# Kernel optimization log

Measured on AMD Instinct MI355X. Metric: run time of the kernel, lower is better.

## Reference

```python
import jax, jax.numpy as jnp
import numpy as np

SCALES = (1, 3, 7, 15)
EPS_LN = 1e-5

def _layernorm(x, g, b):
    mu = jnp.mean(x, axis=-1, keepdims=True)
    var = jnp.mean(jnp.square(x - mu), axis=-1, keepdims=True)
    return (x - mu) / jnp.sqrt(var + EPS_LN) * g + b

def setup_inputs() -> dict:
    key = jax.random.key(0)
    ks = jax.random.split(key, 6)
    B, L, H, NL = 8, 4096, 1024, 4
    s = 0.02
    return {
        "sequence_features": jax.random.normal(ks[0], (B, L, H), jnp.float32),
        "hierarchy_masks": jax.random.uniform(ks[1], (B, L, NL), jnp.float32),
        "level_embeddings": jax.random.normal(ks[2], (NL, H), jnp.float32) * s,
        "lt_w": jax.random.normal(ks[3], (H, H), jnp.float32) * (1.0 / np.sqrt(H)),
        "lt_b": jnp.zeros((H,), jnp.float32),
        "ln1_g": jnp.ones((H,), jnp.float32),
        "ln1_b": jnp.zeros((H,), jnp.float32),
        "ft_w": jax.random.normal(ks[4], (H, H), jnp.float32) * (1.0 / np.sqrt(H)),
        "ft_b": jnp.zeros((H,), jnp.float32),
        "ln2_g": jnp.ones((H,), jnp.float32),
        "ln2_b": jnp.zeros((H,), jnp.float32),
    }

def _hierarchical_fusion(t, masks, level_emb, temperature=1.0):
    # t: [B,L,H], masks: [B,L,NL], level_emb: [NL,H]
    H = t.shape[-1]
    scores = jnp.einsum('blh,nh->bln', t, level_emb) / temperature      # [B,L,NL]
    keep = masks > 0.5
    w = jnp.where(keep, jnp.exp(scores), 0.0)                            # masked exp weights
    tot = jnp.sum(w, axis=-1, keepdims=True)                             # [B,L,1]
    fused = jnp.einsum('bln,nh->blh', w, level_emb)
    fused = jnp.where(tot > 1e-8, fused / jnp.where(tot > 1e-8, tot, 1.0), fused)
    gate = jax.nn.sigmoid(jnp.sum(fused * t, axis=-1, keepdims=True) / H)
    return gate * fused + (1.0 - gate) * t

def _multi_scale(x):
    # x: [B,L,H]; variable-window mean per scale via prefix sums
    B, L, H = x.shape
    csum = jnp.concatenate([jnp.zeros((B, 1, H), x.dtype), jnp.cumsum(x, axis=1)], axis=1)  # [B,L+1,H]
    pos = jnp.arange(L)
    agg = jnp.zeros_like(x)
    for scale in SCALES:
        start = jnp.clip(pos - scale // 2, 0, L)
        end = jnp.clip(pos + scale // 2 + 1, 0, L)
        wsum = jnp.take(csum, end, axis=1) - jnp.take(csum, start, axis=1)  # [B,L,H]
        cnt = (end - start).astype(x.dtype)[None, :, None]
        sw = 1.0 / (1.0 + np.log(float(scale)))
        agg = agg + sw * (wsum / cnt)
    return agg

def reference(sequence_features, hierarchy_masks, level_embeddings, lt_w, lt_b,
              ln1_g, ln1_b, ft_w, ft_b, ln2_g, ln2_b):
    t = _layernorm(sequence_features @ lt_w + lt_b, ln1_g, ln1_b)
    fused = _hierarchical_fusion(t, hierarchy_masks, level_embeddings)
    agg = _multi_scale(fused)
    out = _layernorm(agg @ ft_w + ft_b, ln2_g, ln2_b)
    return out + sequence_features
```

## Files before the change

### kernel.cpp

```cpp
#include <hip/hip_runtime.h>
#include <stdint.h>

typedef unsigned short u16;
typedef unsigned int u32;
typedef u16 u16x8 __attribute__((ext_vector_type(8)));
typedef u16 u16x4 __attribute__((ext_vector_type(4)));
typedef u16 u16x2 __attribute__((ext_vector_type(2)));
typedef __bf16 bf16x8 __attribute__((ext_vector_type(8)));
typedef float f32x4 __attribute__((ext_vector_type(4)));

__device__ __forceinline__ float bf2f(u16 u) {
    unsigned int x = ((unsigned int)u) << 16;
    float f; __builtin_memcpy(&f, &x, 4); return f;
}
__device__ __forceinline__ u16 f2bf(float f) {
    unsigned int x; __builtin_memcpy(&x, &f, 4);
    x += 0x7fffu + ((x >> 16) & 1u);
    return (u16)(x >> 16);
}
__device__ __forceinline__ float wsum(float v) {
#pragma unroll
    for (int o = 32; o > 0; o >>= 1) v += __shfl_xor(v, o, 64);
    return v;
}

__device__ __forceinline__ void gload16(const void* g, void* l) {
    const __attribute__((address_space(1))) u32* gp =
        reinterpret_cast<const __attribute__((address_space(1))) u32*>(
            reinterpret_cast<uintptr_t>(g));
    __attribute__((address_space(3))) u32* lp =
        reinterpret_cast<__attribute__((address_space(3))) u32*>(
            reinterpret_cast<uintptr_t>(l));
    __builtin_amdgcn_global_load_lds(gp, lp, 16, 0, 0);
}

template<int C_F32>
__global__ __launch_bounds__(256) void gemm_bt(
    const u16* __restrict__ A, const u16* __restrict__ Bt,
    void* __restrict__ Cp, int M, int N, int K)
{
    __shared__ __align__(16) u16 sA[128 * 32];
    __shared__ __align__(16) u16 sB[128 * 32];
    const int t = threadIdx.x;
    const int lane = t & 63, wave = t >> 6;
    const int quad = lane >> 4, lr = lane & 15;

    const int nwg = gridDim.x * gridDim.y;
    int id = blockIdx.y * gridDim.x + blockIdx.x;
    int swz = ((nwg & 7) == 0) ? ((id & 7) * (nwg >> 3) + (id >> 3)) : id;
    const int bx = swz % gridDim.x, by = swz / gridDim.x;
    const int m0 = by * 128, n0 = bx * 128;
    const int wm = (wave & 1) * 64, wn = (wave >> 1) * 64;

    const int r0 = t >> 2, kc = (t & 3) * 8;
    const u16* ga = A + (size_t)(m0 + r0) * K + kc;
    const u16* gb = Bt + (size_t)(n0 + r0) * K + kc;
    u16* la = sA + t * 8;
    u16* lb = sB + t * 8;
    const size_t rstride = (size_t)64 * K;

    f32x4 acc[4][4] = {};

    for (int kt = 0; kt < K; kt += 32) {
        __syncthreads();
        gload16(ga + kt, la);
        gload16(ga + kt + rstride, la + 2048);
        gload16(gb + kt, lb);
        gload16(gb + kt + rstride, lb + 2048);
        __syncthreads();

        bf16x8 af[4], bfr[4];
#pragma unroll
        for (int i = 0; i < 4; ++i)
            af[i] = *(const bf16x8*)(sA + (wm + i * 16 + lr) * 32 + quad * 8);
#pragma unroll
        for (int j = 0; j < 4; ++j)
            bfr[j] = *(const bf16x8*)(sB + (wn + j * 16 + lr) * 32 + quad * 8);
#pragma unroll
        for (int i = 0; i < 4; ++i)
#pragma unroll
            for (int j = 0; j < 4; ++j)
                acc[i][j] = __builtin_amdgcn_mfma_f32_16x16x32_bf16(af[i], bfr[j], acc[i][j], 0, 0, 0);
    }
#pragma unroll
    for (int i = 0; i < 4; ++i) {
        int mrow = m0 + wm + i * 16 + quad * 4;
#pragma unroll
        for (int j = 0; j < 4; ++j) {
            int ncol = n0 + wn + j * 16 + lr;
#pragma unroll
            for (int r = 0; r < 4; ++r) {
                if (C_F32) ((float*)Cp)[(size_t)(mrow + r) * N + ncol] = acc[i][j][r];
                else       ((u16*)Cp)[(size_t)(mrow + r) * N + ncol] = f2bf(acc[i][j][r]);
            }
        }
    }
}

__global__ __launch_bounds__(256) void f32_to_bf16(
    const float* __restrict__ in, u16* __restrict__ out, int n8)
{
    int i = blockIdx.x * 256 + threadIdx.x;
    const int stride = gridDim.x * 256;
    for (; i < n8; i += stride) {
        f32x4 a = *(const f32x4*)(in + (size_t)i * 8);
        f32x4 b = *(const f32x4*)(in + (size_t)i * 8 + 4);
        u16x8 o;
#pragma unroll
        for (int p = 0; p < 4; ++p) { o[p] = f2bf(a[p]); o[p + 4] = f2bf(b[p]); }
        *(u16x8*)(out + (size_t)i * 8) = o;
    }
}

__global__ __launch_bounds__(256) void w_transpose(
    const float* __restrict__ W, u16* __restrict__ Bt, int K, int N)
{
    __shared__ u16 tile[64][72];
    const int t = threadIdx.x;
    const int c4 = (t & 15) * 4;
    const int r0 = t >> 4;
    const int kb = blockIdx.y * 64, nb = blockIdx.x * 64;
#pragma unroll
    for (int p = 0; p < 4; ++p) {
        int k = p * 16 + r0;
        f32x4 v = *(const f32x4*)(W + (size_t)(kb + k) * N + nb + c4);
        u16x4 o;
#pragma unroll
        for (int j = 0; j < 4; ++j) o[j] = f2bf(v[j]);
        *(u16x4*)&tile[k][c4] = o;
    }
    __syncthreads();
#pragma unroll
    for (int p = 0; p < 4; ++p) {
        int n = p * 16 + r0;
        u16x4 o;
#pragma unroll
        for (int j = 0; j < 4; ++j) o[j] = tile[c4 + j][n];
        *(u16x4*)(Bt + (size_t)(nb + n) * K + kb + c4) = o;
    }
}

__global__ __launch_bounds__(256) void ln1_fusion(
    const u16* Y, const float* __restrict__ ltb,
    const float* __restrict__ g1, const float* __restrict__ b1,
    const float* __restrict__ masks, const float* __restrict__ emb,
    u16* fused, int ROWS)
{
    const int lane = threadIdx.x & 63;
    const int wid = blockIdx.x * (blockDim.x >> 6) + (threadIdx.x >> 6);
    const int nw = gridDim.x * (blockDim.x >> 6);
    const int h0 = lane * 16;

    float ltbv[16], gv[16], bv[16], ev[4][16];
#pragma unroll
    for (int i = 0; i < 16; ++i) {
        ltbv[i] = ltb[h0 + i];
        gv[i] = g1[h0 + i];
        bv[i] = b1[h0 + i];
    }
#pragma unroll
    for (int n = 0; n < 4; ++n)
#pragma unroll
        for (int i = 0; i < 16; ++i) ev[n][i] = emb[n * 1024 + h0 + i];

    for (int r = wid; r < ROWS; r += nw) {
        const u16* yrow = Y + (size_t)r * 1024 + h0;
        u16x8 v0 = *(const u16x8*)(yrow);
        u16x8 v1 = *(const u16x8*)(yrow + 8);
        float y[16], s = 0.f, sq = 0.f;
#pragma unroll
        for (int i = 0; i < 8; ++i) { y[i] = bf2f(v0[i]) + ltbv[i]; y[i + 8] = bf2f(v1[i]) + ltbv[i + 8]; }
#pragma unroll
        for (int i = 0; i < 16; ++i) { s += y[i]; sq += y[i] * y[i]; }
        s = wsum(s); sq = wsum(sq);
        float mu = s * (1.f / 1024.f);
        float var = fmaxf(sq * (1.f / 1024.f) - mu * mu, 0.f);
        float rinv = rsqrtf(var + 1e-5f);
        float tv[16];
#pragma unroll
        for (int i = 0; i < 16; ++i) tv[i] = (y[i] - mu) * rinv * gv[i] + bv[i];

        float p0 = 0.f, p1 = 0.f, p2 = 0.f, p3 = 0.f;
#pragma unroll
        for (int i = 0; i < 16; ++i) {
            p0 += tv[i] * ev[0][i]; p1 += tv[i] * ev[1][i];
            p2 += tv[i] * ev[2][i]; p3 += tv[i] * ev[3][i];
        }
        p0 = wsum(p0); p1 = wsum(p1); p2 = wsum(p2); p3 = wsum(p3);
        p0 = fminf(p0, 30.f); p1 = fminf(p1, 30.f); p2 = fminf(p2, 30.f); p3 = fminf(p3, 30.f);

        f32x4 mk = *(const f32x4*)(masks + (size_t)r * 4);
        float w0 = mk[0] > 0.5f ? expf(p0) : 0.f;
        float w1 = mk[1] > 0.5f ? expf(p1) : 0.f;
        float w2 = mk[2] > 0.5f ? expf(p2) : 0.f;
        float w3 = mk[3] > 0.5f ? expf(p3) : 0.f;
        float tot = w0 + w1 + w2 + w3;
        float inv = tot > 1e-8f ? 1.f / tot : 1.f;

        float fu[16], d = 0.f;
#pragma unroll
        for (int i = 0; i < 16; ++i) {
            fu[i] = (w0 * ev[0][i] + w1 * ev[1][i] + w2 * ev[2][i] + w3 * ev[3][i]) * inv;
            d += fu[i] * tv[i];
        }
        d = wsum(d);
        float gate = 1.f / (1.f + expf(fminf(-d * (1.f / 1024.f), 30.f)));

        u16x8 o0, o1;
#pragma unroll
        for (int i = 0; i < 8; ++i) {
            o0[i] = f2bf(gate * fu[i] + (1.f - gate) * tv[i]);
            o1[i] = f2bf(gate * fu[i + 8] + (1.f - gate) * tv[i + 8]);
        }
        u16* orow = fused + (size_t)r * 1024 + h0;
        *(u16x8*)(orow) = o0;
        *(u16x8*)(orow + 8) = o1;
    }
}

#define MS_SEG 64
#define MS_HH 512
#define MS_ROWS (MS_SEG + 14)
__global__ __launch_bounds__(256) void multiscale_slide(
    const u16* __restrict__ fused, u16* __restrict__ agg, int L)
{
    __shared__ __align__(16) u16 sT[MS_ROWS * MS_HH];
    const int t = threadIdx.x;
    const int lane = t & 63, wave = t >> 6;
    const int hhalf = blockIdx.x & 1;
    const int bseg = blockIdx.x >> 1;
    const int nseg = L / MS_SEG;
    const int b = bseg / nseg, seg = bseg - b * nseg;
    const int l0 = seg * MS_SEG;
    const size_t base = (size_t)b * L * 1024 + (size_t)hhalf * MS_HH;

    for (int r = wave; r < MS_ROWS; r += 4) {
        int gl = l0 + r - 7;
        u16x8 v = {};
        if ((unsigned)gl < (unsigned)L)
            v = *(const u16x8*)(fused + base + (size_t)gl * 1024 + lane * 8);
        *(u16x8*)(sT + r * MS_HH + lane * 8) = v;
    }
    __syncthreads();

    const int h0 = lane * 8;
    const int lq = wave;
    const u16* rowp = sT + (lq * 16) * MS_HH + h0;

#define LOADR(dst, rr) { u16x8 _v = *(const u16x8*)(rowp + (rr) * MS_HH); \
    _Pragma("unroll") for (int e = 0; e < 8; ++e) dst[e] = bf2f(_v[e]); }

    float fc[8], a3[8], a7[8], a15[8];
    {
        float u[8], v[8];
        LOADR(fc, 7);
        LOADR(u, 6); LOADR(v, 8);
#pragma unroll
        for (int e = 0; e < 8; ++e) a3[e] = fc[e] + u[e] + v[e];
        LOADR(u, 5); LOADR(v, 9);
#pragma unroll
        for (int e = 0; e < 8; ++e) a7[e] = a3[e] + u[e] + v[e];
        LOADR(u, 4); LOADR(v, 10);
#pragma unroll
        for (int e = 0; e < 8; ++e) a7[e] += u[e] + v[e];
        LOADR(u, 3); LOADR(v, 11);
#pragma unroll
        for (int e = 0; e < 8; ++e) a15[e] = a7[e] + u[e] + v[e];
        LOADR(u, 2); LOADR(v, 12);
#pragma unroll
        for (int e = 0; e < 8; ++e) a15[e] += u[e] + v[e];
        LOADR(u, 1); LOADR(v, 13);
#pragma unroll
        for (int e = 0; e < 8; ++e) a15[e] += u[e] + v[e];
        LOADR(u, 0); LOADR(v, 14);
#pragma unroll
        for (int e = 0; e < 8; ++e) a15[e] += u[e] + v[e];
    }

    const float SW1 = 1.f / (1.f + logf(3.f));
    const float SW2 = 1.f / (1.f + logf(7.f));
    const float SW3 = 1.f / (1.f + logf(15.f));
    const float C1 = SW1 / 3.f, C2 = SW2 / 7.f, C3 = SW3 / 15.f;

    u16* outp = agg + base + (size_t)(l0 + lq * 16) * 1024 + h0;
#pragma unroll
    for (int i = 0; i < 16; ++i) {
        const int l = l0 + lq * 16 + i;
        float c1 = C1, c2 = C2, c3 = C3;
        if (l < 7 || l + 7 >= L) {
            int s1 = l - 1 < 0 ? 0 : l - 1, e1 = l + 2 > L ? L : l + 2;
            int s2 = l - 3 < 0 ? 0 : l - 3, e2 = l + 4 > L ? L : l + 4;
            int s3 = l - 7 < 0 ? 0 : l - 7, e3 = l + 8 > L ? L : l + 8;
            c1 = SW1 / (float)(e1 - s1);
            c2 = SW2 / (float)(e2 - s2);
            c3 = SW3 / (float)(e3 - s3);
        }
        u16x8 o;
#pragma unroll
        for (int e = 0; e < 8; ++e)
            o[e] = f2bf(fc[e] + c1 * a3[e] + c2 * a7[e] + c3 * a15[e]);
        *(u16x8*)(outp + (size_t)i * 1024) = o;

        if (i < 15) {
            float p1[8], p2[8], m1[8], p4[8], m3[8], p8[8], m7[8];
            LOADR(p1, 7 + i + 1); LOADR(p2, 7 + i + 2); LOADR(m1, 7 + i - 1);
            LOADR(p4, 7 + i + 4); LOADR(m3, 7 + i - 3);
            LOADR(p8, 7 + i + 8); LOADR(m7, 7 + i - 7);
#pragma unroll
            for (int e = 0; e < 8; ++e) {
                a3[e]  += p2[e] - m1[e];
                a7[e]  += p4[e] - m3[e];
                a15[e] += p8[e] - m7[e];
                fc[e]   = p1[e];
            }
        }
    }
#undef LOADR
}

#define BM 128
#define BN 128
#define BKK 32
#define SBS (BN + 2)
__global__ __launch_bounds__(256) void gemm_k_bf_f32(
    const u16* __restrict__ Ap, const float* __restrict__ B,
    float* __restrict__ Cp, int M, int N, int K)
{
    __shared__ __align__(16) u16 sA[BM * BKK];
    __shared__ __align__(16) u16 sB[BKK * SBS];
    const int t = threadIdx.x;
    const int lane = t & 63, wave = t >> 6;
    const int m0 = blockIdx.y * BM, n0 = blockIdx.x * BN;
    const int wm = (wave & 1) * 64, wn = (wave >> 1) * 64;
    const int quad = lane >> 4, lr = lane & 15;

    f32x4 acc[4][4] = {};

    for (int kt = 0; kt < K; kt += BKK) {
        u16x8 va[2], vb[2];
#pragma unroll
        for (int r = 0; r < 2; ++r) {
            int c = t + r * 256;
            int arow = c >> 2, aks = (c & 3) * 8;
            va[r] = *(const u16x8*)(Ap + (size_t)(m0 + arow) * K + kt + aks);
            int bk = c >> 4, bn = (c & 15) * 8;
            const float* gb = B + (size_t)(kt + bk) * N + n0 + bn;
            f32x4 g0 = *(const f32x4*)gb;
            f32x4 g1 = *(const f32x4*)(gb + 4);
#pragma unroll
            for (int p = 0; p < 4; ++p) { vb[r][p] = f2bf(g0[p]); vb[r][p + 4] = f2bf(g1[p]); }
        }
        __syncthreads();
#pragma unroll
        for (int r = 0; r < 2; ++r) {
            int c = t + r * 256;
            *(u16x8*)((char*)sA + (size_t)c * 16) = va[r];
            int bk = c >> 4, bn = (c & 15) * 8;
            u16* dst = sB + bk * SBS + bn;
#pragma unroll
            for (int p = 0; p < 4; ++p) {
                u16x2 w; w[0] = vb[r][2 * p]; w[1] = vb[r][2 * p + 1];
                *(u16x2*)(dst + 2 * p) = w;
            }
        }
        __syncthreads();

        bf16x8 af[4], bfr[4];
#pragma unroll
        for (int i = 0; i < 4; ++i)
            af[i] = *(const bf16x8*)((const char*)sA + (wm + i * 16 + lr) * 64 + quad * 16);
#pragma unroll
        for (int i = 0; i < 4; ++i) {
            u16 tmp[8];
#pragma unroll
            for (int j = 0; j < 8; ++j)
                tmp[j] = sB[(quad * 8 + j) * SBS + (wn + i * 16 + lr)];
            __builtin_memcpy(&bfr[i], tmp, 16);
        }
#pragma unroll
        for (int i = 0; i < 4; ++i)
#pragma unroll
            for (int j = 0; j < 4; ++j)
                acc[i][j] = __builtin_amdgcn_mfma_f32_16x16x32_bf16(af[i], bfr[j], acc[i][j], 0, 0, 0);
    }
#pragma unroll
    for (int i = 0; i < 4; ++i) {
        int mrow = m0 + wm + i * 16 + quad * 4;
#pragma unroll
        for (int j = 0; j < 4; ++j) {
            int ncol = n0 + wn + j * 16 + lr;
#pragma unroll
            for (int r = 0; r < 4; ++r)
                Cp[(size_t)(mrow + r) * N + ncol] = acc[i][j][r];
        }
    }
}

__global__ __launch_bounds__(256) void ln2_res(
    float* Y, const float* __restrict__ ftb,
    const float* __restrict__ g2, const float* __restrict__ b2,
    const float* __restrict__ x, int ROWS)
{
    const int lane = threadIdx.x & 63;
    const int wid = blockIdx.x * (blockDim.x >> 6) + (threadIdx.x >> 6);
    const int nw = gridDim.x * (blockDim.x >> 6);
    const int h0 = lane * 16;

    float ftbv[16], gv[16], bv[16];
#pragma unroll
    for (int i = 0; i < 16; ++i) {
        ftbv[i] = ftb[h0 + i];
        gv[i] = g2[h0 + i];
        bv[i] = b2[h0 + i];
    }
    for (int r = wid; r < ROWS; r += nw) {
        float* yrow = Y + (size_t)r * 1024 + h0;
        float y[16], s = 0.f, sq = 0.f;
#pragma unroll
        for (int q = 0; q < 4; ++q) {
            f32x4 v = *(const f32x4*)(yrow + 4 * q);
#pragma unroll
            for (int p = 0; p < 4; ++p) y[4 * q + p] = v[p] + ftbv[4 * q + p];
        }
#pragma unroll
        for (int i = 0; i < 16; ++i) { s += y[i]; sq += y[i] * y[i]; }
        s = wsum(s); sq = wsum(sq);
        float mu = s * (1.f / 1024.f);
        float var = fmaxf(sq * (1.f / 1024.f) - mu * mu, 0.f);
        float rinv = rsqrtf(var + 1e-5f);

        const float* xrow = x + (size_t)r * 1024 + h0;
#pragma unroll
        for (int q = 0; q < 4; ++q) {
            f32x4 xv = *(const f32x4*)(xrow + 4 * q);
            f32x4 o;
#pragma unroll
            for (int p = 0; p < 4; ++p)
                o[p] = (y[4 * q + p] - mu) * rinv * gv[4 * q + p] + bv[4 * q + p] + xv[p];
            *(f32x4*)(yrow + 4 * q) = o;
        }
    }
}

extern "C" void kernel_launch(void* const* d_in, const int* in_sizes, int n_in,
                              void* d_out, int out_size, void* d_ws, size_t ws_size,
                              hipStream_t stream) {
    const float* x     = (const float*)d_in[0];
    const float* masks = (const float*)d_in[1];
    const float* emb   = (const float*)d_in[2];
    const float* ltw   = (const float*)d_in[3];
    const float* ltb   = (const float*)d_in[4];
    const float* g1    = (const float*)d_in[5];
    const float* b1    = (const float*)d_in[6];
    const float* ftw   = (const float*)d_in[7];
    const float* ftb   = (const float*)d_in[8];
    const float* g2    = (const float*)d_in[9];
    const float* b2    = (const float*)d_in[10];
    float* out = (float*)d_out;

    const int H = 1024, L = 4096;
    const int M = in_sizes[0] / H;
    const size_t MB = 1024 * 1024;

    u16* plane0 = (u16*)d_out;
    u16* xbf    = (u16*)((char*)d_out + 64 * MB);
    u16* aggP   = (u16*)d_ws;
    const bool roomy = ws_size >= 68 * MB;
    u16* Bt1 = roomy ? (u16*)((char*)d_ws + 64 * MB) : (u16*)d_ws;
    u16* Bt2 = roomy ? (u16*)((char*)d_ws + 66 * MB) : nullptr;

    f32_to_bf16<<<2048, 256, 0, stream>>>(x, xbf, M * H / 8);
    w_transpose<<<dim3(16, 16), 256, 0, stream>>>(ltw, Bt1, H, H);
    if (roomy) w_transpose<<<dim3(16, 16), 256, 0, stream>>>(ftw, Bt2, H, H);

    gemm_bt<0><<<dim3(H / 128, M / 128), 256, 0, stream>>>(xbf, Bt1, plane0, M, H, H);
    ln1_fusion<<<1024, 256, 0, stream>>>(plane0, ltb, g1, b1, masks, emb, plane0, M);
    multiscale_slide<<<(M / MS_SEG) * 2, 256, 0, stream>>>(plane0, aggP, L);
    if (roomy)
        gemm_bt<1><<<dim3(H / 128, M / 128), 256, 0, stream>>>(aggP, Bt2, out, M, H, H);
    else
        gemm_k_bf_f32<<<dim3(H / BN, M / BM), 256, 0, stream>>>(aggP, ftw, out, M, H, H);
    ln2_res<<<1024, 256, 0, stream>>>(out, ftb, g2, b2, x, M);
}
```

Measured before the change: 586.3 us.

## Fuse second GEMM with LayerNorm2 and residual into one full-row kernel

Adds a GEMM kernel where each block computes 64 full rows (all 1024 columns) and then applies bias, LayerNorm statistics via shuffle and shared-memory reduction, the affine transform and the residual add in its epilogue. This removes the fp32 round trip of the GEMM output and the separate ln2_res launch. The trade-off is a large B tile in LDS (64KB) reloaded by every block with no double buffering, only 512 blocks, and heavy accumulator register use, all of which may hurt GEMM efficiency.

```diff
diff --git a/kernel.cpp b/kernel.cpp
--- a/kernel.cpp
+++ b/kernel.cpp
@@ -95,6 +95,108 @@
             }
         }
     }
+}
+
+__global__ __launch_bounds__(512) void gemm2_ln2(
+    const u16* __restrict__ A, const u16* __restrict__ Bt,
+    const float* __restrict__ x, float* __restrict__ out,
+    const float* __restrict__ ftb, const float* __restrict__ g2,
+    const float* __restrict__ b2, int M, int K)
+{
+    __shared__ __align__(16) u16 sB[1024 * 32];
+    __shared__ __align__(16) u16 sA[64 * 32];
+    __shared__ float sStat[64][9];
+    const int t = threadIdx.x;
+    const int lane = t & 63, wave = t >> 6;
+    const int quad = lane >> 4, lr = lane & 15;
+    const int wm = (wave >> 2) * 32;
+    const int wn = (wave & 3) * 256;
+    const int m0 = blockIdx.x * 64;
+
+    const int brow = t >> 2, kc = (t & 3) * 8;
+    const u16* gb = Bt + (size_t)brow * K + kc;
+    u16* lb = sB + t * 8;
+    const u16* ga = A + (size_t)(m0 + brow) * K + kc;
+    u16* la = sA + t * 8;
+
+    f32x4 acc[2][16] = {};
+
+    for (int kt = 0; kt < K; kt += 32) {
+        __syncthreads();
+#pragma unroll
+        for (int r = 0; r < 8; ++r)
+            gload16(gb + (size_t)r * 128 * K + kt, lb + r * 4096);
+        if (wave < 4)
+            gload16(ga + kt, la);
+        __syncthreads();
+
+        bf16x8 af0 = *(const bf16x8*)(sA + (wm + 0 * 16 + lr) * 32 + quad * 8);
+        bf16x8 af1 = *(const bf16x8*)(sA + (wm + 1 * 16 + lr) * 32 + quad * 8);
+#pragma unroll
+        for (int j = 0; j < 16; ++j) {
+            bf16x8 bf = *(const bf16x8*)(sB + (wn + j * 16 + lr) * 32 + quad * 8);
+            acc[0][j] = __builtin_amdgcn_mfma_f32_16x16x32_bf16(af0, bf, acc[0][j], 0, 0, 0);
+            acc[1][j] = __builtin_amdgcn_mfma_f32_16x16x32_bf16(af1, bf, acc[1][j], 0, 0, 0);
+        }
+    }
+
+    float fv[16], gv[16], bv[16];
+#pragma unroll
+    for (int j = 0; j < 16; ++j) {
+        int col = wn + j * 16 + lr;
+        fv[j] = ftb[col]; gv[j] = g2[col]; bv[j] = b2[col];
+    }
+
+    float ps[2][4], pq[2][4];
+#pragma unroll
+    for (int i = 0; i < 2; ++i)
+#pragma unroll
+        for (int r = 0; r < 4; ++r) {
+            float s = 0.f, q = 0.f;
+#pragma unroll
+            for (int j = 0; j < 16; ++j) {
+                float y = acc[i][j][r] + fv[j];
+                s += y; q += y * y;
+            }
+#pragma unroll
+            for (int o = 8; o > 0; o >>= 1) {
+                s += __shfl_xor(s, o, 64);
+                q += __shfl_xor(q, o, 64);
+            }
+            ps[i][r] = s; pq[i][r] = q;
+        }
+
+    __syncthreads();
+    if (lr == 0) {
+#pragma unroll
+        for (int i = 0; i < 2; ++i)
+#pragma unroll
+            for (int r = 0; r < 4; ++r) {
+                int row = wm + i * 16 + quad * 4 + r;
+                sStat[row][(wave & 3) * 2 + 0] = ps[i][r];
+                sStat[row][(wave & 3) * 2 + 1] = pq[i][r];
+            }
+    }
+    __syncthreads();
+
+#pragma unroll
+    for (int i = 0; i < 2; ++i)
+#pragma unroll
+        for (int r = 0; r < 4; ++r) {
+            int row = wm + i * 16 + quad * 4 + r;
+            float S  = sStat[row][0] + sStat[row][2] + sStat[row][4] + sStat[row][6];
+            float SQ = sStat[row][1] + sStat[row][3] + sStat[row][5] + sStat[row][7];
+            float mu = S * (1.f / 1024.f);
+            float var = fmaxf(SQ * (1.f / 1024.f) - mu * mu, 0.f);
+            float rinv = rsqrtf(var + 1e-5f);
+            const size_t grow = (size_t)(m0 + row) * 1024;
+#pragma unroll
+            for (int j = 0; j < 16; ++j) {
+                int col = wn + j * 16 + lr;
+                float y = acc[i][j][r] + fv[j];
+                out[grow + col] = (y - mu) * rinv * gv[j] + bv[j] + x[grow + col];
+            }
+        }
 }
 
 __global__ __launch_bounds__(256) void f32_to_bf16(
@@ -476,9 +578,10 @@
     gemm_bt<0><<<dim3(H / 128, M / 128), 256, 0, stream>>>(xbf, Bt1, plane0, M, H, H);
     ln1_fusion<<<1024, 256, 0, stream>>>(plane0, ltb, g1, b1, masks, emb, plane0, M);
     multiscale_slide<<<(M / MS_SEG) * 2, 256, 0, stream>>>(plane0, aggP, L);
-    if (roomy)
-        gemm_bt<1><<<dim3(H / 128, M / 128), 256, 0, stream>>>(aggP, Bt2, out, M, H, H);
-    else
+    if (roomy) {
+        gemm2_ln2<<<M / 64, 512, 0, stream>>>(aggP, Bt2, x, out, ftb, g2, b2, M, H);
+    } else {
         gemm_k_bf_f32<<<dim3(H / BN, M / BM), 256, 0, stream>>>(aggP, ftw, out, M, H, H);
-    ln2_res<<<1024, 256, 0, stream>>>(out, ftb, g2, b2, x, M);
-}
+        ln2_res<<<1024, 256, 0, stream>>>(out, ftb, g2, b2, x, M);
+    }
+}
```

Measured after the change: 598.1 us. +2.0%, slower.
